# Kernel optimization log

Hardware: AMD Instinct MI355X
Metric: run time of the kernel (lower is better)

## Reference

```python
import jax, jax.numpy as jnp
import numpy as np

D_MODEL = 1024
N_HEADS = 16
ALPHA = 0.7
C_PARAM = 5
CUTOFF = C_PARAM // 2 + 1  # 3
LN_EPS = 1e-12
B, S = 4, 2048


def setup_inputs() -> dict:
    key = jax.random.key(0)
    ks = jax.random.split(key, 10)
    d = D_MODEL
    scale = 1.0 / np.sqrt(d)
    return {
        "input_tensor": jax.random.normal(ks[0], (B, S, d), dtype=jnp.float32),
        "attention_mask": jnp.ones((1, 1, S, S), dtype=jnp.int32),
        "sqrt_beta": jax.random.normal(ks[1], (1, 1, d), dtype=jnp.float32),
        "ln_gamma": jnp.ones((d,), dtype=jnp.float32),
        "ln_beta": jnp.zeros((d,), dtype=jnp.float32),
        "q_w": jax.random.normal(ks[2], (d, d), dtype=jnp.float32) * scale,
        "q_b": jnp.zeros((d,), dtype=jnp.float32),
        "k_w": jax.random.normal(ks[3], (d, d), dtype=jnp.float32) * scale,
        "k_b": jnp.zeros((d,), dtype=jnp.float32),
        "v_w": jax.random.normal(ks[4], (d, d), dtype=jnp.float32) * scale,
        "v_b": jnp.zeros((d,), dtype=jnp.float32),
    }


def _layer_norm(x, g, b):
    mu = jnp.mean(x, axis=-1, keepdims=True)
    var = jnp.mean(jnp.square(x - mu), axis=-1, keepdims=True)
    return (x - mu) * jax.lax.rsqrt(var + LN_EPS) * g + b


def bsarec_layer(x, mask, sqrt_beta, ln_gamma, ln_beta, q_w, q_b, k_w, k_b, v_w, v_b):
    batch, seq_len, hidden = x.shape
    # ---- FrequencyLayer (DSP branch) ----
    xf = jnp.fft.rfft(x, axis=1, norm='ortho')                 # [B, S//2+1, D]
    freq = jnp.arange(xf.shape[1])[None, :, None]
    low_pass = jnp.fft.irfft(jnp.where(freq < CUTOFF, xf, 0.0), n=seq_len, axis=1, norm='ortho')
    high_pass = x - low_pass
    seq_fft = low_pass + jnp.square(sqrt_beta) * high_pass
    dsp = _layer_norm(seq_fft + x, ln_gamma, ln_beta)          # dropout=0 -> identity
    # ---- MultiHeadAttention (GSP branch) ----
    h, d_k = N_HEADS, hidden // N_HEADS
    def split(t):  # [B,S,D] -> [B,H,S,d_k]
        return t.reshape(batch, seq_len, h, d_k).transpose(0, 2, 1, 3)
    q = split(x @ q_w.T + q_b)
    k = split(x @ k_w.T + k_b)
    v = split(x @ v_w.T + v_b)
    scores = jnp.einsum('bhsd,bhtd->bhst', q, k) / jnp.sqrt(jnp.float32(d_k))
    scores = jnp.where(mask == 0, -jnp.inf, scores)
    scores = scores - jnp.max(scores)                           # global max, as in source
    p = jax.nn.softmax(scores, axis=-1)
    p = jnp.where(jnp.isnan(p), 0.0, p)
    out = jnp.einsum('bhst,bhtd->bhsd', p, v)
    gsp = out.transpose(0, 2, 1, 3).reshape(batch, seq_len, hidden)
    return ALPHA * dsp + (1.0 - ALPHA) * gsp


def reference(input_tensor, attention_mask, sqrt_beta, ln_gamma, ln_beta, q_w, q_b, k_w, k_b, v_w, v_b):
    return bsarec_layer(input_tensor, attention_mask, sqrt_beta, ln_gamma, ln_beta,
                        q_w, q_b, k_w, k_b, v_w, v_b)
```

## Files before the change

kernel.cpp:

```cpp
#include <hip/hip_runtime.h>

#define S_LEN 2048
#define DM 1024
#define NB 4
#define NROWS (NB * S_LEN)
#define NHEADS 16
#define DK 64

typedef __bf16 bf16x8 __attribute__((ext_vector_type(8)));
typedef __bf16 bf16x2 __attribute__((ext_vector_type(2)));
typedef float f32x4 __attribute__((ext_vector_type(4)));
typedef float f32x2 __attribute__((ext_vector_type(2)));
typedef unsigned u32x4 __attribute__((ext_vector_type(4)));

struct __align__(8) us4 { unsigned short x, y, z, w; };

__device__ __forceinline__ unsigned cvt2(float a, float b) {
    f32x2 t; t.x = a; t.y = b;
    bf16x2 h = __builtin_convertvector(t, bf16x2);
    return __builtin_bit_cast(unsigned, h);
}
__device__ __forceinline__ unsigned short f2bf(float f) {
    __bf16 h = (__bf16)f;
    return __builtin_bit_cast(unsigned short, h);
}

__device__ __forceinline__ void gl2lds16(const void* g, void* l) {
    __builtin_amdgcn_global_load_lds(
        (const __attribute__((address_space(1))) unsigned int*)g,
        (__attribute__((address_space(3))) unsigned int*)l, 16, 0, 0);
}

#if __has_builtin(__builtin_amdgcn_exp2f)
#define EXP2F(x) __builtin_amdgcn_exp2f(x)
#else
#define EXP2F(x) exp2f(x)
#endif

__global__ __launch_bounds__(256) void prep(
    const float* __restrict__ x, float* __restrict__ coef,
    unsigned short* __restrict__ xbf, const float* __restrict__ qw,
    const float* __restrict__ kw, const float* __restrict__ vw,
    unsigned short* __restrict__ wbf) {
    int bx = blockIdx.x;
    if (bx >= 512) {
        int idx = ((bx - 512) * 256 + threadIdx.x) * 2;
        int which = idx >> 20, off = idx & 0xFFFFF;
        const float* src = (which == 0) ? qw : ((which == 1) ? kw : vw);
        float2 v = *(const float2*)(&src[off]);
        *(unsigned*)(&wbf[idx]) = cvt2(v.x, v.y);
        return;
    }
    int b = bx >> 7, dc = (bx >> 5) & 3, tc = bx & 31;
    int d = dc * 256 + threadIdx.x;
    __shared__ float tw[4][64];
    if (threadIdx.x < 64) {
        const float omega = 6.283185307179586476925f / (float)S_LEN;
        float sn, cs;
        __sincosf(omega * (float)(tc * 64 + threadIdx.x), &sn, &cs);
        tw[0][threadIdx.x] = sn;
        tw[1][threadIdx.x] = cs;
        tw[2][threadIdx.x] = 2.f * sn * cs;
        tw[3][threadIdx.x] = cs * cs - sn * sn;
    }
    __syncthreads();
    float c0 = 0.f, c1 = 0.f, s1 = 0.f, c2 = 0.f, s2 = 0.f;
    for (int i = 0; i < 64; ++i) {
        int t = tc * 64 + i;
        long idx = (long)(b * S_LEN + t) * DM + d;
        float v = x[idx];
        xbf[idx] = f2bf(v);
        c0 += v;
        c1 += v * tw[1][i];
        s1 += v * tw[0][i];
        c2 += v * tw[3][i];
        s2 += v * tw[2][i];
    }
    int base = b * DM + d;
    atomicAdd(&coef[0 * 4096 + base], c0);
    atomicAdd(&coef[1 * 4096 + base], c1);
    atomicAdd(&coef[2 * 4096 + base], s1);
    atomicAdd(&coef[3 * 4096 + base], c2);
    atomicAdd(&coef[4 * 4096 + base], s2);
}

__global__ __launch_bounds__(256) void dsp_ln(
    const float* __restrict__ x, const float* __restrict__ coef,
    const float* __restrict__ sqrt_beta, const float* __restrict__ gamma,
    const float* __restrict__ beta, const unsigned short* __restrict__ Og,
    float* __restrict__ out) {
    int row = blockIdx.x;
    int b = row >> 11, t = row & (S_LEN - 1);
    int tid = threadIdx.x, lane = tid & 63, wave = tid >> 6;
    const float omega = 6.283185307179586476925f / (float)S_LEN;
    float sn, cs;
    __sincosf(omega * (float)t, &sn, &cs);
    float c2t = cs * cs - sn * sn, s2t = 2.f * sn * cs;
    int d0 = tid * 4;
    long base = (long)row * DM;
    float4 xv = *(const float4*)(&x[base + d0]);
    int cb = b * DM + d0;
    float4 C0 = *(const float4*)(&coef[0 * 4096 + cb]);
    float4 C1 = *(const float4*)(&coef[1 * 4096 + cb]);
    float4 S1 = *(const float4*)(&coef[2 * 4096 + cb]);
    float4 C2 = *(const float4*)(&coef[3 * 4096 + cb]);
    float4 S2 = *(const float4*)(&coef[4 * 4096 + cb]);
    float4 sb = *(const float4*)(&sqrt_beta[d0]);
    const float inv_s = 1.0f / (float)S_LEN;
    float y[4];
#pragma unroll
    for (int i = 0; i < 4; ++i) {
        float c0 = (&C0.x)[i], c1 = (&C1.x)[i], s1 = (&S1.x)[i],
              c2 = (&C2.x)[i], s2 = (&S2.x)[i];
        float lp = (c0 + 2.f * (c1 * cs + s1 * sn) + 2.f * (c2 * c2t + s2 * s2t)) * inv_s;
        float xx = (&xv.x)[i];
        float b2 = (&sb.x)[i];
        b2 = b2 * b2;
        y[i] = xx + lp + b2 * (xx - lp);
    }
    float ssum = y[0] + y[1] + y[2] + y[3];
    float ssq = y[0] * y[0] + y[1] * y[1] + y[2] * y[2] + y[3] * y[3];
#pragma unroll
    for (int m = 1; m < 64; m <<= 1) {
        ssum += __shfl_xor(ssum, m, 64);
        ssq += __shfl_xor(ssq, m, 64);
    }
    __shared__ float red[8];
    if (lane == 0) { red[wave] = ssum; red[4 + wave] = ssq; }
    __syncthreads();
    float S = red[0] + red[1] + red[2] + red[3];
    float SQ = red[4] + red[5] + red[6] + red[7];
    float mu = S * (1.0f / DM);
    float var = SQ * (1.0f / DM) - mu * mu;
    float rstd = rsqrtf(var + 1e-12f);
    float4 g = *(const float4*)(&gamma[d0]);
    float4 be = *(const float4*)(&beta[d0]);
    us4 gv = *(const us4*)(&Og[((long)((b << 4) + (d0 >> 6)) * S_LEN + t) * DK + (d0 & 63)]);
    const unsigned short* gp = (const unsigned short*)&gv;
    float4 o;
#pragma unroll
    for (int i = 0; i < 4; ++i)
        (&o.x)[i] = 0.7f * ((y[i] - mu) * rstd * (&g.x)[i] + (&be.x)[i]) +
                    0.3f * __uint_as_float((unsigned)gp[i] << 16);
    *(float4*)(&out[base + d0]) = o;
}

__global__ __launch_bounds__(512, 2) void gemm_qkv(
    const unsigned short* __restrict__ A, const unsigned short* __restrict__ W,
    const float* __restrict__ qb, const float* __restrict__ kb,
    const float* __restrict__ vb, unsigned short* __restrict__ Qo,
    unsigned short* __restrict__ Ko, unsigned short* __restrict__ Vt_g) {
    const int m0 = blockIdx.y * 256;
    const int n0g = blockIdx.x * 256;
    const int which = n0g >> 10;
    const int n0 = n0g & 1023;
    const int tid = threadIdx.x;
    const int lane = tid & 63, wave = tid >> 6;
    const int wm = wave >> 2, wn = wave & 3;
    const int r = lane & 15, q = lane >> 4;
    __shared__ __align__(16) unsigned short SmF[4 * 16384];
    const int scol = ((lane & 3) ^ ((lane >> 3) & 3)) * 8;
    const int rs = (q ^ ((r >> 1) & 3)) * 8;
    f32x4 acc[8][4] = {};

#define GST(slot_, kt_)                                                     \
    do {                                                                    \
        const int ko_ = (kt_) * 32;                                         \
        _Pragma("unroll")                                                   \
        for (int e = 0; e < 2; ++e) {                                       \
            int cA = e * 8 + wave;                                          \
            int grow = cA * 16 + (lane >> 2);                               \
            gl2lds16(&A[(long)(m0 + grow) * DM + ko_ + scol],               \
                     &SmF[(slot_) * 16384 + cA * 512 + lane * 8]);          \
            gl2lds16(&W[(long)(n0g + grow) * DM + ko_ + scol],              \
                     &SmF[(slot_) * 16384 + 8192 + cA * 512 + lane * 8]);   \
        }                                                                   \
    } while (0)

    GST(0, 0);
    GST(1, 1);
    asm volatile("s_waitcnt vmcnt(4)" ::: "memory");
    __builtin_amdgcn_s_barrier();

    for (int kti = 0; kti < 32; ++kti) {
        const int slot = kti & 3;
        if (kti < 30) GST((kti + 2) & 3, kti + 2);
        const unsigned short* Ac = &SmF[slot * 16384];
        const unsigned short* Bc = Ac + 8192;
        bf16x8 bfr[4];
#pragma unroll
        for (int ni = 0; ni < 4; ++ni)
            bfr[ni] = *(const bf16x8*)(&Bc[(wn * 64 + ni * 16 + r) * 32 + rs]);
        __builtin_amdgcn_s_setprio(1);
#pragma unroll
        for (int mh = 0; mh < 2; ++mh) {
            bf16x8 af[4];
#pragma unroll
            for (int i = 0; i < 4; ++i)
                af[i] = *(const bf16x8*)(
                    &Ac[(wm * 128 + (mh * 4 + i) * 16 + r) * 32 + rs]);
#pragma unroll
            for (int i = 0; i < 4; ++i)
#pragma unroll
                for (int ni = 0; ni < 4; ++ni)
                    acc[mh * 4 + i][ni] = __builtin_amdgcn_mfma_f32_16x16x32_bf16(
                        af[i], bfr[ni], acc[mh * 4 + i][ni], 0, 0, 0);
        }
        __builtin_amdgcn_s_setprio(0);
        if (kti < 31) {
            if (kti < 30) {
                asm volatile("s_waitcnt vmcnt(4)" ::: "memory");
            } else {
                asm volatile("s_waitcnt vmcnt(0)" ::: "memory");
            }
            __builtin_amdgcn_s_barrier();
        }
    }
#undef GST
    __syncthreads();

    const float* bias = (which == 0) ? qb : ((which == 1) ? kb : vb);
    if (which < 2) {
        const float qs = (which == 0) ? 0.18033688011112042f : 1.0f;
        unsigned short* Out = (which == 0) ? Qo : Ko;
#pragma unroll
        for (int strip = 0; strip < 2; ++strip) {
            if (strip) __syncthreads();
            if (wm == strip) {
#pragma unroll
                for (int mi = 0; mi < 8; ++mi) {
                    int row = mi * 16 + q * 4;
#pragma unroll
                    for (int ni = 0; ni < 4; ++ni) {
                        int col = wn * 64 + ni * 16 + r;
                        float bv = bias[n0 + col];
#pragma unroll
                        for (int reg = 0; reg < 4; ++reg)
                            SmF[(row + reg) * 264 + col] =
                                f2bf((acc[mi][ni][reg] + bv) * qs);
                    }
                }
            }
            __syncthreads();
#pragma unroll
            for (int p = 0; p < 8; ++p) {
                int row = p * 16 + wave * 2 + (lane >> 5);
                int cc = (lane & 31) * 8;
                uint4 v = *(const uint4*)(&SmF[row * 264 + cc]);
                long gb = (long)(m0 + strip * 128 + row) * DM + n0 + cc;
                *(uint4*)(&Out[gb]) = v;
            }
        }
    } else {
        const int bb = m0 >> 11, sg = m0 & (S_LEN - 1);
#pragma unroll
        for (int strip = 0; strip < 2; ++strip) {
            if (strip) __syncthreads();
            if (wm == strip) {
#pragma unroll
                for (int ni = 0; ni < 4; ++ni) {
                    int col = wn * 64 + ni * 16 + r;
                    float bv = bias[n0 + col];
#pragma unroll
                    for (int mi = 0; mi < 8; ++mi) {
                        int row = mi * 16 + q * 4;
                        *(unsigned*)(&SmF[col * 136 + row]) =
                            cvt2(acc[mi][ni][0] + bv, acc[mi][ni][1] + bv);
                        *(unsigned*)(&SmF[col * 136 + row + 2]) =
                            cvt2(acc[mi][ni][2] + bv, acc[mi][ni][3] + bv);
                    }
                }
            }
            __syncthreads();
#pragma unroll
            for (int p = 0; p < 8; ++p) {
                int n = p * 32 + wave * 4 + (lane >> 4);
                int mcc = (lane & 15) * 8;
                uint4 v = *(const uint4*)(&SmF[n * 136 + mcc]);
                long gb = ((long)bb * DM + n0 + n) * S_LEN + sg + strip * 128 + mcc;
                *(uint4*)(&Vt_g[gb]) = v;
            }
        }
    }
}

__global__ __launch_bounds__(256, 2) void attn(
    const unsigned short* __restrict__ Q, const unsigned short* __restrict__ K,
    const unsigned short* __restrict__ Vt_g, unsigned short* __restrict__ Og) {
    int bx = blockIdx.x;
    int bh = bx & 63, qt = bx >> 6;
    int b = bh >> 4, h = bh & 15;
    const int tid = threadIdx.x, lane = tid & 63, wave = tid >> 6;
    const int r = lane & 15, q = lane >> 4;
    const int hc = h * DK;
    const int q0 = qt * 256 + wave * 64;

    bf16x8 aq[4][2];
#pragma unroll
    for (int mt = 0; mt < 4; ++mt) {
        long rowQ = (long)(b * S_LEN + q0 + mt * 16 + r) * DM + hc;
        aq[mt][0] = *(const bf16x8*)(&Q[rowQ + q * 8]);
        aq[mt][1] = *(const bf16x8*)(&Q[rowQ + 32 + q * 8]);
    }

    __shared__ __align__(16) unsigned short Ks[2][4096];
    __shared__ __align__(16) unsigned short Vt[2][4096];
    __shared__ float denL[256];

    f32x4 accO[4][4] = {};
    float den[4] = {};

    const int lr = lane >> 3, lc = lane & 7;
    const int cw0 = wave * 2, cw1 = cw0 + 1;
    const int ld0 = cw0 * 512, ld1 = cw1 * 512;
    const int row0 = cw0 * 8 + lr, row1 = cw1 * 8 + lr;
    const int cg0 = lc ^ lr;
    const int cg1 = lc ^ lr ^ 4;
    const unsigned short* kp0 = K + (long)(b * S_LEN + row0) * DM + hc + cg0 * 8;
    const unsigned short* kp1 = K + (long)(b * S_LEN + row1) * DM + hc + cg1 * 8;
    const unsigned short* vp0 = Vt_g + (long)(bh * 64 + row0) * S_LEN + cg0 * 8;
    const unsigned short* vp1 = Vt_g + (long)(bh * 64 + row1) * S_LEN + cg1 * 8;

    const int lo = r & 3, hi = r >> 2;
    const int abase = (hi * 8 + lo) * 64;
    const int ca = (q ^ lo ^ ((hi & 1) << 2)) * 8;
    const int cb2 = ca ^ 32;
    const int va0 = (q ^ (r & 7) ^ (((r >> 3) & 1) << 2)) * 8;
    const int va1 = va0 ^ 32;

#define STAGE(buf)                                    \
    do {                                              \
        gl2lds16(kp0, &Ks[buf][ld0 + lane * 8]);      \
        gl2lds16(kp1, &Ks[buf][ld1 + lane * 8]);      \
        gl2lds16(vp0, &Vt[buf][ld0 + lane * 8]);      \
        gl2lds16(vp1, &Vt[buf][ld1 + lane * 8]);      \
        kp0 += 64 * DM; kp1 += 64 * DM; vp0 += 64; vp1 += 64; \
    } while (0)

    STAGE(0);
    asm volatile("s_waitcnt vmcnt(0)" ::: "memory");
    __builtin_amdgcn_s_barrier();

    for (int t = 0; t < 32; ++t) {
        const int cur = t & 1;
        if (t < 31) STAGE(cur ^ 1);
        const unsigned short* Kc = Ks[cur];
        const unsigned short* Vc = Vt[cur];
        __builtin_amdgcn_s_setprio(1);
#pragma unroll
        for (int c = 0; c < 2; ++c) {
            const int cb64 = c * 2048;
            bf16x8 ak00 = *(const bf16x8*)(&Kc[cb64 + abase + ca]);
            bf16x8 ak01 = *(const bf16x8*)(&Kc[cb64 + abase + cb2]);
            bf16x8 ak10 = *(const bf16x8*)(&Kc[cb64 + 256 + abase + cb2]);
            bf16x8 ak11 = *(const bf16x8*)(&Kc[cb64 + 256 + abase + ca]);
            const int va = c ? va1 : va0;
            bf16x8 bv[4];
            bv[0] = *(const bf16x8*)(&Vc[(0 * 16 + r) * 64 + va]);
            bv[1] = *(const bf16x8*)(&Vc[(1 * 16 + r) * 64 + va]);
            bv[2] = *(const bf16x8*)(&Vc[(2 * 16 + r) * 64 + va]);
            bv[3] = *(const bf16x8*)(&Vc[(3 * 16 + r) * 64 + va]);
#pragma unroll
            for (int mt = 0; mt < 4; ++mt) {
                f32x4 sa = {}, sb = {};
                sa = __builtin_amdgcn_mfma_f32_16x16x32_bf16(ak00, aq[mt][0], sa, 0, 0, 0);
                sa = __builtin_amdgcn_mfma_f32_16x16x32_bf16(ak01, aq[mt][1], sa, 0, 0, 0);
                sb = __builtin_amdgcn_mfma_f32_16x16x32_bf16(ak10, aq[mt][0], sb, 0, 0, 0);
                sb = __builtin_amdgcn_mfma_f32_16x16x32_bf16(ak11, aq[mt][1], sb, 0, 0, 0);
                float p0 = EXP2F(sa[0]), p1 = EXP2F(sa[1]);
                float p2 = EXP2F(sa[2]), p3 = EXP2F(sa[3]);
                float p4 = EXP2F(sb[0]), p5 = EXP2F(sb[1]);
                float p6 = EXP2F(sb[2]), p7 = EXP2F(sb[3]);
                den[mt] += ((p0 + p1) + (p2 + p3)) + ((p4 + p5) + (p6 + p7));
                u32x4 wv;
                wv.x = cvt2(p0, p1); wv.y = cvt2(p2, p3);
                wv.z = cvt2(p4, p5); wv.w = cvt2(p6, p7);
                bf16x8 ap = __builtin_bit_cast(bf16x8, wv);
#pragma unroll
                for (int dt = 0; dt < 4; ++dt)
                    accO[mt][dt] = __builtin_amdgcn_mfma_f32_16x16x32_bf16(
                        ap, bv[dt], accO[mt][dt], 0, 0, 0);
            }
        }
        __builtin_amdgcn_s_setprio(0);
        asm volatile("s_waitcnt vmcnt(0)" ::: "memory");
        __builtin_amdgcn_s_barrier();
    }
#undef STAGE

#pragma unroll
    for (int mt = 0; mt < 4; ++mt) {
        float d = den[mt];
        d += __shfl_xor(d, 16, 64);
        d += __shfl_xor(d, 32, 64);
        if (q == 0) denL[wave * 64 + mt * 16 + r] = d;
    }
#pragma unroll
    for (int mt = 0; mt < 4; ++mt) {
        float4 dv = *(const float4*)(&denL[wave * 64 + mt * 16 + q * 4]);
        float rs[4];
#pragma unroll
        for (int reg = 0; reg < 4; ++reg) rs[reg] = 1.0f / (&dv.x)[reg];
        long obase = (long)bh * S_LEN + q0 + mt * 16 + q * 4;
#pragma unroll
        for (int dt = 0; dt < 4; ++dt) {
            int col = dt * 16 + r;
#pragma unroll
            for (int reg = 0; reg < 4; ++reg)
                Og[(obase + reg) * DK + col] = f2bf(accO[mt][dt][reg] * rs[reg]);
        }
    }
}

extern "C" void kernel_launch(void* const* d_in, const int* in_sizes, int n_in,
                              void* d_out, int out_size, void* d_ws, size_t ws_size,
                              hipStream_t stream) {
    const float* x = (const float*)d_in[0];
    const float* sqrt_beta = (const float*)d_in[2];
    const float* gamma = (const float*)d_in[3];
    const float* beta = (const float*)d_in[4];
    const float* qw = (const float*)d_in[5];
    const float* qb = (const float*)d_in[6];
    const float* kw = (const float*)d_in[7];
    const float* kb = (const float*)d_in[8];
    const float* vw = (const float*)d_in[9];
    const float* vb = (const float*)d_in[10];
    float* out = (float*)d_out;

    char* ws = (char*)d_ws;
    float* coef = (float*)ws;
    unsigned short* xbf = (unsigned short*)(ws + 81920);
    unsigned short* wbf = (unsigned short*)(ws + 81920 + 16777216);
    unsigned short* Qb = (unsigned short*)(ws + 81920 + 16777216 + 6291456);
    unsigned short* Kb = Qb + (long)NROWS * DM;
    unsigned short* Vt_g = Kb + (long)NROWS * DM;
    unsigned short* Og = xbf;

    hipMemsetAsync(coef, 0, 5 * 4096 * sizeof(float), stream);
    prep<<<6656, 256, 0, stream>>>(x, coef, xbf, qw, kw, vw, wbf);
    dim3 ggrid(3 * DM / 256, NROWS / 256);
    gemm_qkv<<<ggrid, 512, 0, stream>>>(xbf, wbf, qb, kb, vb, Qb, Kb, Vt_g);
    attn<<<NB * NHEADS * (S_LEN / 256), 256, 0, stream>>>(Qb, Kb, Vt_g, Og);
    dsp_ln<<<NROWS, 256, 0, stream>>>(x, coef, sqrt_beta, gamma, beta, Og, out);
}
```

Measured before the change: 267.2 us.

## Split QKV GEMM k-step into two phases interleaving loads with MFMA

Restructures the QKV GEMM main loop into two half-phases. Each phase loads one half of the A fragments from LDS and issues half of the next tile's global-to-LDS copies, then synchronises with barriers and runs 16 MFMAs under raised priority. This is meant to spread memory issue across the compute so LDS reads and global loads overlap better with matrix math across waves, in a ping-pong style schedule. The cost is extra barriers per iteration, which may add stall time.

```diff
diff --git a/kernel.cpp b/kernel.cpp
--- a/kernel.cpp
+++ b/kernel.cpp
@@ -163,60 +163,71 @@
     const int rs = (q ^ ((r >> 1) & 3)) * 8;
     f32x4 acc[8][4] = {};
 
-#define GST(slot_, kt_)                                                     \
+#define GSTH(slot_, kt_, e_)                                                \
     do {                                                                    \
         const int ko_ = (kt_) * 32;                                         \
-        _Pragma("unroll")                                                   \
-        for (int e = 0; e < 2; ++e) {                                       \
-            int cA = e * 8 + wave;                                          \
-            int grow = cA * 16 + (lane >> 2);                               \
-            gl2lds16(&A[(long)(m0 + grow) * DM + ko_ + scol],               \
-                     &SmF[(slot_) * 16384 + cA * 512 + lane * 8]);          \
-            gl2lds16(&W[(long)(n0g + grow) * DM + ko_ + scol],              \
-                     &SmF[(slot_) * 16384 + 8192 + cA * 512 + lane * 8]);   \
-        }                                                                   \
+        int cA = (e_) * 8 + wave;                                           \
+        int grow = cA * 16 + (lane >> 2);                                   \
+        gl2lds16(&A[(long)(m0 + grow) * DM + ko_ + scol],                   \
+                 &SmF[(slot_) * 16384 + cA * 512 + lane * 8]);              \
+        gl2lds16(&W[(long)(n0g + grow) * DM + ko_ + scol],                  \
+                 &SmF[(slot_) * 16384 + 8192 + cA * 512 + lane * 8]);       \
     } while (0)
 
-    GST(0, 0);
-    GST(1, 1);
+    GSTH(0, 0, 0); GSTH(0, 0, 1);
+    GSTH(1, 1, 0); GSTH(1, 1, 1);
     asm volatile("s_waitcnt vmcnt(4)" ::: "memory");
     __builtin_amdgcn_s_barrier();
 
     for (int kti = 0; kti < 32; ++kti) {
         const int slot = kti & 3;
-        if (kti < 30) GST((kti + 2) & 3, kti + 2);
         const unsigned short* Ac = &SmF[slot * 16384];
         const unsigned short* Bc = Ac + 8192;
-        bf16x8 bfr[4];
+        bf16x8 bfr[4], af[4];
 #pragma unroll
         for (int ni = 0; ni < 4; ++ni)
             bfr[ni] = *(const bf16x8*)(&Bc[(wn * 64 + ni * 16 + r) * 32 + rs]);
+#pragma unroll
+        for (int i = 0; i < 4; ++i)
+            af[i] = *(const bf16x8*)(&Ac[(wm * 128 + i * 16 + r) * 32 + rs]);
+        if (kti < 30) GSTH((kti + 2) & 3, kti + 2, 0);
+        __builtin_amdgcn_sched_barrier(0);
+        __builtin_amdgcn_s_barrier();
+        asm volatile("s_waitcnt lgkmcnt(0)" ::: "memory");
+        __builtin_amdgcn_sched_barrier(0);
         __builtin_amdgcn_s_setprio(1);
 #pragma unroll
-        for (int mh = 0; mh < 2; ++mh) {
-            bf16x8 af[4];
-#pragma unroll
-            for (int i = 0; i < 4; ++i)
-                af[i] = *(const bf16x8*)(
-                    &Ac[(wm * 128 + (mh * 4 + i) * 16 + r) * 32 + rs]);
-#pragma unroll
-            for (int i = 0; i < 4; ++i)
-#pragma unroll
-                for (int ni = 0; ni < 4; ++ni)
-                    acc[mh * 4 + i][ni] = __builtin_amdgcn_mfma_f32_16x16x32_bf16(
-                        af[i], bfr[ni], acc[mh * 4 + i][ni], 0, 0, 0);
+        for (int i = 0; i < 4; ++i)
+#pragma unroll
+            for (int ni = 0; ni < 4; ++ni)
+                acc[i][ni] = __builtin_amdgcn_mfma_f32_16x16x32_bf16(
+                    af[i], bfr[ni], acc[i][ni], 0, 0, 0);
+        __builtin_amdgcn_s_setprio(0);
+        __builtin_amdgcn_s_barrier();
+#pragma unroll
+        for (int i = 0; i < 4; ++i)
+            af[i] = *(const bf16x8*)(&Ac[(wm * 128 + (4 + i) * 16 + r) * 32 + rs]);
+        if (kti < 30) GSTH((kti + 2) & 3, kti + 2, 1);
+        __builtin_amdgcn_sched_barrier(0);
+        __builtin_amdgcn_s_barrier();
+        asm volatile("s_waitcnt lgkmcnt(0)" ::: "memory");
+        __builtin_amdgcn_sched_barrier(0);
+        __builtin_amdgcn_s_setprio(1);
+#pragma unroll
+        for (int i = 0; i < 4; ++i)
+#pragma unroll
+            for (int ni = 0; ni < 4; ++ni)
+                acc[4 + i][ni] = __builtin_amdgcn_mfma_f32_16x16x32_bf16(
+                    af[i], bfr[ni], acc[4 + i][ni], 0, 0, 0);
+        __builtin_amdgcn_s_setprio(0);
+        if (kti < 30) {
+            asm volatile("s_waitcnt vmcnt(4)" ::: "memory");
+        } else if (kti == 30) {
+            asm volatile("s_waitcnt vmcnt(0)" ::: "memory");
         }
-        __builtin_amdgcn_s_setprio(0);
-        if (kti < 31) {
-            if (kti < 30) {
-                asm volatile("s_waitcnt vmcnt(4)" ::: "memory");
-            } else {
-                asm volatile("s_waitcnt vmcnt(0)" ::: "memory");
-            }
-            __builtin_amdgcn_s_barrier();
-        }
-    }
-#undef GST
+        __builtin_amdgcn_s_barrier();
+    }
+#undef GSTH
     __syncthreads();
 
     const float* bias = (which == 0) ? qb : ((which == 1) ? kb : vb);
```

Result: slower. 275.0 us (+2.9%).
